# Performance work log

Hardware: AMD Instinct MI355X
Metric: run time of the kernel (lower is better)

Reference implementation:

```python
import jax, jax.numpy as jnp
import numpy as np

B, H, S, D = 512, 1024, 1024, 128
TOPK = 32

def setup_inputs() -> dict:
    key = jax.random.key(0)
    ks = jax.random.split(key, 12)
    w = lambda k, shape: (jax.random.normal(k, shape, dtype=jnp.float32) * 0.02)
    return {
        "latent": jax.random.normal(ks[0], (B, H), dtype=jnp.float32),
        "memory": jax.random.normal(ks[1], (B, S, D), dtype=jnp.float32),
        "read_query_w": w(ks[2], (H, D)),
        "read_query_b": jnp.zeros((D,), jnp.float32),
        "memory_key": w(ks[3], (S, D)),
        "write_gate_w": w(ks[4], (H + D, 1)),
        "write_gate_b": jnp.zeros((1,), jnp.float32),
        "dmd_proj_w": w(ks[5], (H + D, 1)),
        "dmd_proj_b": jnp.zeros((1,), jnp.float32),
        "phase_proj_w": w(ks[6], (H, 1)),
        "phase_proj_b": jnp.zeros((1,), jnp.float32),
        "write_value_w": w(ks[7], (H, D)),
        "write_value_b": jnp.zeros((D,), jnp.float32),
    }

def reference(latent, memory, read_query_w, read_query_b, memory_key,
              write_gate_w, write_gate_b, dmd_proj_w, dmd_proj_b,
              phase_proj_w, phase_proj_b, write_value_w, write_value_b):
    # soft read over memory slots
    query = latent @ read_query_w + read_query_b              # [B, D]
    logits = jnp.einsum('bd,sd->bs', query, memory_key)       # [B, S]
    weights = jax.nn.softmax(logits, axis=-1)
    # top-k masked renormalization (topk=32 < S)
    _, topk_idx = jax.lax.top_k(weights, TOPK)                # [B, K]
    rows = jnp.arange(weights.shape[0])[:, None]
    mask = jnp.zeros_like(weights).at[rows, topk_idx].set(1.0)
    weights = weights * mask
    weights = weights / jnp.clip(weights.sum(-1, keepdims=True), 1e-8)
    read = jnp.einsum('bs,bsd->bd', weights, memory)          # [B, D]
    gate_input = jnp.concatenate([latent, read], axis=-1)     # [B, H+D]
    # sigmoid gate (gating_mode='sigmoid')
    gate = jax.nn.sigmoid(gate_input @ write_gate_w + write_gate_b)  # [B, 1]
    # dmd gating
    dmd_signal = jnp.tanh(gate_input @ dmd_proj_w + dmd_proj_b)
    gate = jnp.clip(gate * (0.75 + 0.5 * (dmd_signal + 1.0) * 0.5), 0.0, 1.0)
    # phase gating
    phase = latent @ phase_proj_w + phase_proj_b
    gate = gate * (0.5 * (1.0 + jnp.cos(phase)))
    # soft scatter-write update
    value = (latent @ write_value_w + write_value_b)[:, None, :]      # [B, 1, D]
    gw = gate[:, :, None] * weights[:, :, None]                       # [B, S, 1]
    new_memory = (1.0 - gw) * memory + gw * value                     # [B, S, D]
    return read, new_memory, weights
```

## Files before the change

### kernel.cpp

```cpp
#include <hip/hip_runtime.h>
#include <math.h>

#define NB 512
#define NH 1024
#define NS 1024
#define ND 128
#define NK 32

typedef float fx4 __attribute__((ext_vector_type(4)));

__global__ __launch_bounds__(512, 4) void fused_kernel(
    const float* __restrict__ latent,
    const float* __restrict__ memory,
    const float* __restrict__ rq_w,
    const float* __restrict__ rq_b,
    const float* __restrict__ mem_key,
    const float* __restrict__ wg_w,
    const float* __restrict__ wg_b,
    const float* __restrict__ dmd_w,
    const float* __restrict__ dmd_b,
    const float* __restrict__ ph_w,
    const float* __restrict__ ph_b,
    const float* __restrict__ wv_w,
    const float* __restrict__ wv_b,
    float* __restrict__ out_read,
    float* __restrict__ out_mem,
    float* __restrict__ out_wts)
{
  const int b    = blockIdx.x;
  const int tid  = threadIdx.x;
  const int lane = tid & 63;
  const int wv   = tid >> 6;

  __shared__ float lat[NH];
  __shared__ float wfull[NS];
  __shared__ float part[512];
  __shared__ __align__(16) float qv[ND];
  __shared__ float rd[ND];
  __shared__ float tvw[256];
  __shared__ int   tiw[256];
  __shared__ float wkL[NK];
  __shared__ int   tiL[NK];
  __shared__ __align__(16) float valw_s[ND];
  __shared__ float gred[24];
  __shared__ float scal[1];

  const fx4* __restrict__ msrc = (const fx4*)memory + (size_t)b * (NS * ND / 4);
  fx4*       __restrict__ mdst = (fx4*)out_mem      + (size_t)b * (NS * ND / 4);
  fx4 buf[8];
  int cur = 0;

#define CK_LOAD(N)  { _Pragma("unroll") \
    for (int j = 0; j < (N); ++j) \
      buf[j] = __builtin_nontemporal_load(msrc + (size_t)(cur + j) * 512 + tid); }
#define CK_STORE(N) { _Pragma("unroll") \
    for (int j = 0; j < (N); ++j) \
      __builtin_nontemporal_store(buf[j], mdst + (size_t)(cur + j) * 512 + tid); \
    cur += (N); }

  CK_LOAD(8);
  lat[tid]       = latent[(size_t)b * NH + tid];
  lat[tid + 512] = latent[(size_t)b * NH + tid + 512];
  CK_STORE(8);
  __syncthreads();

  CK_LOAD(4);
  {
    const int d = tid & 127, p = tid >> 7;
    const float* W = rq_w + (size_t)(p * 256) * ND + d;
    const float* L = lat + p * 256;
    float acc = 0.f;
    #pragma unroll 8
    for (int h = 0; h < 256; ++h) acc = fmaf(L[h], W[(size_t)h * ND], acc);
    part[tid] = acc;
  }
  CK_STORE(4);
  __syncthreads();

  CK_LOAD(8);
  if (tid < ND)
    qv[tid] = part[tid] + part[tid + 128] + part[tid + 256] + part[tid + 384] + rq_b[tid];
  CK_STORE(8);
  __syncthreads();

  float r0 = 0.f, r1 = 0.f;
  CK_LOAD(4);
  {
    const float4* q4 = (const float4*)qv;
    const float4* k0 = (const float4*)(mem_key + (size_t)tid * ND);
    const float4* k1 = (const float4*)(mem_key + (size_t)(tid + 512) * ND);
    #pragma unroll 8
    for (int i = 0; i < ND / 4; ++i) {
      float4 q = q4[i];
      float4 x = k0[i];
      float4 y = k1[i];
      r0 += q.x * x.x + q.y * x.y + q.z * x.z + q.w * x.w;
      r1 += q.x * y.x + q.y * y.y + q.z * y.z + q.w * y.w;
    }
  }
  CK_STORE(4);

  const float NEGINF = -3.0e38f;
  float selv = NEGINF; int seli = -1; float wkreg = 0.f;
  CK_LOAD(4);
  {
    const int s0 = tid, s1 = tid + 512;
    float v0 = r0, v1 = r1;
    for (int kk = 0; kk < NK; ++kk) {
      float best; int bi;
      if (v0 >= v1) { best = v0; bi = s0; } else { best = v1; bi = s1; }
      #pragma unroll
      for (int off = 1; off < 64; off <<= 1) {
        float ov = __shfl_xor(best, off);
        int   oi = __shfl_xor(bi, off);
        if (ov > best || (ov == best && oi < bi)) { best = ov; bi = oi; }
      }
      if (lane == 0) { tvw[(wv << 5) + kk] = best; tiw[(wv << 5) + kk] = bi; }
      if (bi == s0) v0 = NEGINF;
      if (bi == s1) v1 = NEGINF;
    }
  }
  wfull[tid] = 0.f; wfull[tid + 512] = 0.f;
  CK_STORE(4);
  __syncthreads();

  CK_LOAD(8);
  if (wv == 0) {
    float m0 = tvw[lane], m1 = tvw[lane + 64], m2 = tvw[lane + 128], m3 = tvw[lane + 192];
    int   i0 = tiw[lane], i1 = tiw[lane + 64], i2 = tiw[lane + 128], i3 = tiw[lane + 192];
    for (int kk = 0; kk < NK; ++kk) {
      float best = m0; int bi = i0;
      if (m1 > best || (m1 == best && i1 < bi)) { best = m1; bi = i1; }
      if (m2 > best || (m2 == best && i2 < bi)) { best = m2; bi = i2; }
      if (m3 > best || (m3 == best && i3 < bi)) { best = m3; bi = i3; }
      #pragma unroll
      for (int off = 1; off < 64; off <<= 1) {
        float ov = __shfl_xor(best, off);
        int   oi = __shfl_xor(bi, off);
        if (ov > best || (ov == best && oi < bi)) { best = ov; bi = oi; }
      }
      if (kk == lane) { selv = best; seli = bi; }
      if (bi == i0) m0 = NEGINF;
      if (bi == i1) m1 = NEGINF;
      if (bi == i2) m2 = NEGINF;
      if (bi == i3) m3 = NEGINF;
    }
    float maxv = __shfl(selv, 0);
    float e = (lane < NK) ? expf(selv - maxv) : 0.f;
    float s = e;
    #pragma unroll
    for (int off = 1; off < 64; off <<= 1) s += __shfl_xor(s, off);
    wkreg = e / s;
    if (lane < NK) { wkL[lane] = wkreg; tiL[lane] = seli; }
  }
  CK_STORE(8);
  __syncthreads();

  if (wv == 0 && lane < NK) wfull[seli] = wkreg;
  CK_LOAD(4);
  {
    const int d = tid & 127, p = tid >> 7;
    const float* mb = memory + (size_t)b * NS * ND;
    float racc = 0.f;
    #pragma unroll
    for (int k = p * 8; k < p * 8 + 8; ++k)
      racc = fmaf(wkL[k], mb[(size_t)tiL[k] * ND + d], racc);
    part[tid] = racc;
  }
  CK_STORE(4);
  __syncthreads();

  CK_LOAD(8);
  if (tid < ND) {
    float r = part[tid] + part[tid + 128] + part[tid + 256] + part[tid + 384];
    rd[tid] = r;
    out_read[(size_t)b * ND + tid] = r;
  }
  CK_STORE(8);
  __syncthreads();

  CK_LOAD(4);
  {
    float l0 = lat[tid], l1 = lat[tid + 512];
    float p1 = l0 * wg_w[tid]  + l1 * wg_w[tid + 512];
    float p2 = l0 * dmd_w[tid] + l1 * dmd_w[tid + 512];
    float p3 = l0 * ph_w[tid]  + l1 * ph_w[tid + 512];
    if (tid < ND) {
      float r = rd[tid];
      p1 += r * wg_w[NH + tid];
      p2 += r * dmd_w[NH + tid];
    }
    #pragma unroll
    for (int off = 1; off < 64; off <<= 1) {
      p1 += __shfl_xor(p1, off);
      p2 += __shfl_xor(p2, off);
      p3 += __shfl_xor(p3, off);
    }
    if (lane == 0) { gred[wv] = p1; gred[8 + wv] = p2; gred[16 + wv] = p3; }
  }
  {
    const int d = tid & 127, p = tid >> 7;
    const float* W = wv_w + (size_t)(p * 256) * ND + d;
    const float* L = lat + p * 256;
    float acc = 0.f;
    #pragma unroll 8
    for (int h = 0; h < 256; ++h) acc = fmaf(L[h], W[(size_t)h * ND], acc);
    part[tid] = acc;
  }
  CK_STORE(4);
  __syncthreads();

  CK_LOAD(6);
  if (tid == 0) {
    float z1 = wg_b[0], z2 = dmd_b[0], z3 = ph_b[0];
    #pragma unroll
    for (int k = 0; k < 8; ++k) { z1 += gred[k]; z2 += gred[8 + k]; z3 += gred[16 + k]; }
    float g  = 1.f / (1.f + expf(-z1));
    float dm = tanhf(z2);
    g = g * (0.75f + 0.25f * (dm + 1.f));
    g = fminf(fmaxf(g, 0.f), 1.f);
    g = g * (0.5f * (1.f + cosf(z3)));
    scal[0] = g;
  }
  CK_STORE(6);
  __syncthreads();

  CK_LOAD(6);
  {
    float w0 = wfull[tid], w1 = wfull[tid + 512];
    out_wts[(size_t)b * NS + tid]       = w0;
    out_wts[(size_t)b * NS + tid + 512] = w1;
    if (tid < ND)
      valw_s[tid] = part[tid] + part[tid + 128] + part[tid + 256] + part[tid + 384] + wv_b[tid];
  }
  CK_STORE(6);
  __syncthreads();

  {
    const float g = scal[0];
    const fx4* v4 = (const fx4*)valw_s;
    #pragma unroll
    for (int u = 0; u < 2; ++u) {
      const int idx = tid + u * 512;
      const int k   = idx >> 5;
      const int c   = idx & 31;
      const float w = g * wkL[k];
      const int row = tiL[k];
      const fx4 m = msrc[(size_t)row * 32 + c];
      __builtin_nontemporal_store((1.f - w) * m + w * v4[c],
                                  mdst + (size_t)row * 32 + c);
    }
  }
#undef CK_LOAD
#undef CK_STORE
}

extern "C" void kernel_launch(void* const* d_in, const int* in_sizes, int n_in,
                              void* d_out, int out_size, void* d_ws, size_t ws_size,
                              hipStream_t stream) {
  const float* latent  = (const float*)d_in[0];
  const float* memory  = (const float*)d_in[1];
  const float* rq_w    = (const float*)d_in[2];
  const float* rq_b    = (const float*)d_in[3];
  const float* mem_key = (const float*)d_in[4];
  const float* wg_w    = (const float*)d_in[5];
  const float* wg_b    = (const float*)d_in[6];
  const float* dmd_w   = (const float*)d_in[7];
  const float* dmd_b   = (const float*)d_in[8];
  const float* ph_w    = (const float*)d_in[9];
  const float* ph_b    = (const float*)d_in[10];
  const float* wv_w    = (const float*)d_in[11];
  const float* wv_b    = (const float*)d_in[12];

  float* out_read = (float*)d_out;
  float* out_mem  = out_read + (size_t)NB * ND;
  float* out_wts  = out_mem + (size_t)NB * NS * ND;

  fused_kernel<<<NB, 512, 0, stream>>>(
      latent, memory, rq_w, rq_b, mem_key, wg_w, wg_b, dmd_w, dmd_b,
      ph_w, ph_b, wv_w, wv_b, out_read, out_mem, out_wts);
}
```

Baseline: 517.0 us.

## Double-buffer memory copy chunks and use LDS-only barriers between phases

Replaces the single register buffer with two ping-pong buffers so each chunk of the memory copy is loaded one phase before it is stored, keeping global loads in flight across compute phases and barriers. __syncthreads is replaced with barriers that wait only on LDS counters, so outstanding global loads and stores do not drain at each phase boundary. A full vmcnt wait is kept before the final scatter write, which preserves ordering with the copied rows. This doubles the register footprint of the copy buffers, which may pressure occupancy under the launch bounds.

```diff
diff --git a/kernel.cpp b/kernel.cpp
--- a/kernel.cpp
+++ b/kernel.cpp
@@ -8,6 +8,17 @@
 #define NK 32
 
 typedef float fx4 __attribute__((ext_vector_type(4)));
+
+__device__ __forceinline__ void bar_lgkm() {
+  asm volatile("s_waitcnt lgkmcnt(0)" ::: "memory");
+  __builtin_amdgcn_s_barrier();
+  __builtin_amdgcn_sched_barrier(0);
+}
+__device__ __forceinline__ void bar_full() {
+  asm volatile("s_waitcnt vmcnt(0) lgkmcnt(0)" ::: "memory");
+  __builtin_amdgcn_s_barrier();
+  __builtin_amdgcn_sched_barrier(0);
+}
 
 __global__ __launch_bounds__(512, 4) void fused_kernel(
     const float* __restrict__ latent,
@@ -47,24 +58,25 @@
 
   const fx4* __restrict__ msrc = (const fx4*)memory + (size_t)b * (NS * ND / 4);
   fx4*       __restrict__ mdst = (fx4*)out_mem      + (size_t)b * (NS * ND / 4);
-  fx4 buf[8];
-  int cur = 0;
-
-#define CK_LOAD(N)  { _Pragma("unroll") \
+  fx4 bufA[8], bufB[8];
+  int cur_l = 0, cur_s = 0;
+
+#define CK_LOAD(BUF, N)  { _Pragma("unroll") \
     for (int j = 0; j < (N); ++j) \
-      buf[j] = __builtin_nontemporal_load(msrc + (size_t)(cur + j) * 512 + tid); }
-#define CK_STORE(N) { _Pragma("unroll") \
+      BUF[j] = __builtin_nontemporal_load(msrc + (size_t)(cur_l + j) * 512 + tid); \
+    cur_l += (N); }
+#define CK_STORE(BUF, N) { _Pragma("unroll") \
     for (int j = 0; j < (N); ++j) \
-      __builtin_nontemporal_store(buf[j], mdst + (size_t)(cur + j) * 512 + tid); \
-    cur += (N); }
-
-  CK_LOAD(8);
+      __builtin_nontemporal_store(BUF[j], mdst + (size_t)(cur_s + j) * 512 + tid); \
+    cur_s += (N); }
+
+  CK_LOAD(bufA, 8);
   lat[tid]       = latent[(size_t)b * NH + tid];
   lat[tid + 512] = latent[(size_t)b * NH + tid + 512];
-  CK_STORE(8);
-  __syncthreads();
-
-  CK_LOAD(4);
+  bar_lgkm();
+
+  CK_LOAD(bufB, 4);
+  CK_STORE(bufA, 8);
   {
     const int d = tid & 127, p = tid >> 7;
     const float* W = rq_w + (size_t)(p * 256) * ND + d;
@@ -74,17 +86,17 @@
     for (int h = 0; h < 256; ++h) acc = fmaf(L[h], W[(size_t)h * ND], acc);
     part[tid] = acc;
   }
-  CK_STORE(4);
-  __syncthreads();
-
-  CK_LOAD(8);
+  bar_lgkm();
+
+  CK_LOAD(bufA, 8);
+  CK_STORE(bufB, 4);
   if (tid < ND)
     qv[tid] = part[tid] + part[tid + 128] + part[tid + 256] + part[tid + 384] + rq_b[tid];
-  CK_STORE(8);
-  __syncthreads();
-
+  bar_lgkm();
+
+  CK_LOAD(bufB, 8);
+  CK_STORE(bufA, 8);
   float r0 = 0.f, r1 = 0.f;
-  CK_LOAD(4);
   {
     const float4* q4 = (const float4*)qv;
     const float4* k0 = (const float4*)(mem_key + (size_t)tid * ND);
@@ -98,11 +110,8 @@
       r1 += q.x * y.x + q.y * y.y + q.z * y.z + q.w * y.w;
     }
   }
-  CK_STORE(4);
-
   const float NEGINF = -3.0e38f;
   float selv = NEGINF; int seli = -1; float wkreg = 0.f;
-  CK_LOAD(4);
   {
     const int s0 = tid, s1 = tid + 512;
     float v0 = r0, v1 = r1;
@@ -121,10 +130,10 @@
     }
   }
   wfull[tid] = 0.f; wfull[tid + 512] = 0.f;
-  CK_STORE(4);
-  __syncthreads();
-
-  CK_LOAD(8);
+  bar_lgkm();
+
+  CK_LOAD(bufA, 8);
+  CK_STORE(bufB, 8);
   if (wv == 0) {
     float m0 = tvw[lane], m1 = tvw[lane + 64], m2 = tvw[lane + 128], m3 = tvw[lane + 192];
     int   i0 = tiw[lane], i1 = tiw[lane + 64], i2 = tiw[lane + 128], i3 = tiw[lane + 192];
@@ -153,11 +162,11 @@
     wkreg = e / s;
     if (lane < NK) { wkL[lane] = wkreg; tiL[lane] = seli; }
   }
-  CK_STORE(8);
-  __syncthreads();
-
+  bar_lgkm();
+
+  CK_LOAD(bufB, 4);
+  CK_STORE(bufA, 8);
   if (wv == 0 && lane < NK) wfull[seli] = wkreg;
-  CK_LOAD(4);
   {
     const int d = tid & 127, p = tid >> 7;
     const float* mb = memory + (size_t)b * NS * ND;
@@ -167,19 +176,19 @@
       racc = fmaf(wkL[k], mb[(size_t)tiL[k] * ND + d], racc);
     part[tid] = racc;
   }
-  CK_STORE(4);
-  __syncthreads();
-
-  CK_LOAD(8);
+  bar_lgkm();
+
+  CK_LOAD(bufA, 8);
+  CK_STORE(bufB, 4);
   if (tid < ND) {
     float r = part[tid] + part[tid + 128] + part[tid + 256] + part[tid + 384];
     rd[tid] = r;
     out_read[(size_t)b * ND + tid] = r;
   }
-  CK_STORE(8);
-  __syncthreads();
-
-  CK_LOAD(4);
+  bar_lgkm();
+
+  CK_LOAD(bufB, 4);
+  CK_STORE(bufA, 8);
   {
     float l0 = lat[tid], l1 = lat[tid + 512];
     float p1 = l0 * wg_w[tid]  + l1 * wg_w[tid + 512];
@@ -207,10 +216,10 @@
     for (int h = 0; h < 256; ++h) acc = fmaf(L[h], W[(size_t)h * ND], acc);
     part[tid] = acc;
   }
-  CK_STORE(4);
-  __syncthreads();
-
-  CK_LOAD(6);
+  bar_lgkm();
+
+  CK_LOAD(bufA, 6);
+  CK_STORE(bufB, 4);
   if (tid == 0) {
     float z1 = wg_b[0], z2 = dmd_b[0], z3 = ph_b[0];
     #pragma unroll
@@ -222,10 +231,10 @@
     g = g * (0.5f * (1.f + cosf(z3)));
     scal[0] = g;
   }
-  CK_STORE(6);
-  __syncthreads();
-
-  CK_LOAD(6);
+  bar_lgkm();
+
+  CK_LOAD(bufB, 6);
+  CK_STORE(bufA, 6);
   {
     float w0 = wfull[tid], w1 = wfull[tid + 512];
     out_wts[(size_t)b * NS + tid]       = w0;
@@ -233,9 +242,10 @@
     if (tid < ND)
       valw_s[tid] = part[tid] + part[tid + 128] + part[tid + 256] + part[tid + 384] + wv_b[tid];
   }
-  CK_STORE(6);
-  __syncthreads();
-
+  bar_lgkm();
+
+  CK_STORE(bufB, 6);
+  bar_full();
   {
     const float g = scal[0];
     const fx4* v4 = (const fx4*)valw_s;
```

Result: no change. 523.2 us (+1.2%).
